# Kernel tuning notes

Measured on AMD Instinct MI355X. Metric: run time of the kernel, lower is better.

## Reference

```python
import jax, jax.numpy as jnp
from jax import lax
import numpy as np

DN = ('NHWC', 'HWIO', 'NHWC')


def conv2(x, w1, b1, w2, b2):
    # Sequential(Conv2D(units,3,same,relu), Conv2D(1,3,same,relu))
    y = jax.nn.relu(lax.conv_general_dilated(x, w1, (1, 1), 'SAME', dimension_numbers=DN) + b1)
    y = jax.nn.relu(lax.conv_general_dilated(y, w2, (1, 1), 'SAME', dimension_numbers=DN) + b2)
    return y


def resize_and_pad(fm, box, Hb, Wb):
    # Static-shape reformulation of tf.image.resize (bilinear, half-pixel) +
    # tf.pad: for every bg pixel inside the box, bilinearly sample the source
    # map; pixels outside the box are zero (the pad region).
    h, w = fm.shape[0], fm.shape[1]
    y_size = jnp.floor(Hb * (box[1] - box[0]))  # int() truncation on positives
    x_size = jnp.floor(Wb * (box[3] - box[2]))
    yf = jnp.floor(Hb * box[0])
    xf = jnp.floor(Wb * box[2])
    Y = jnp.arange(Hb, dtype=fm.dtype)[:, None]
    X = jnp.arange(Wb, dtype=fm.dtype)[None, :]
    ly = Y - yf  # local row inside resized crop
    lx = X - xf
    valid = (ly >= 0) & (ly < y_size) & (lx >= 0) & (lx < x_size)
    sy = jnp.clip((ly + 0.5) * h / jnp.maximum(y_size, 1.0) - 0.5, 0.0, h - 1.0)
    sx = jnp.clip((lx + 0.5) * w / jnp.maximum(x_size, 1.0) - 0.5, 0.0, w - 1.0)
    sy = jnp.broadcast_to(sy, (Hb, Wb))
    sx = jnp.broadcast_to(sx, (Hb, Wb))
    y0 = jnp.floor(sy).astype(jnp.int32)
    x0 = jnp.floor(sx).astype(jnp.int32)
    y1 = jnp.minimum(y0 + 1, h - 1)
    x1 = jnp.minimum(x0 + 1, w - 1)
    wy = (sy - y0.astype(fm.dtype))[..., None]
    wx = (sx - x0.astype(fm.dtype))[..., None]
    top = fm[y0, x0] * (1 - wx) + fm[y0, x1] * wx
    bot = fm[y1, x0] * (1 - wx) + fm[y1, x1] * wx
    out = top * (1 - wy) + bot * wy
    return out * valid[..., None].astype(fm.dtype)


def _forward(instance_feature, bg_feature, bbox, mrcnn_mask,
             w1i, b1i, w2i, b2i, w1b, b1b, w2b, b2b, object_n):
    B, Hi, Wi, C, M = instance_feature.shape
    Hb, Wb = bg_feature.shape[1], bg_feature.shape[2]
    # fold objects into batch for the per-instance conv
    inst = jnp.transpose(instance_feature, (0, 4, 1, 2, 3)).reshape(B * M, Hi, Wi, C)
    inst_w = conv2(inst, w1i, b1i, w2i, b2i)  # [B*M,Hi,Wi,1]
    boxes = jnp.transpose(bbox, (0, 2, 1)).reshape(B * M, 4)
    rp = lambda fm, box: resize_and_pad(fm, box, Hb, Wb)
    rw = jax.vmap(rp)(inst_w, boxes).reshape(B, M, Hb, Wb, 1)      # resized weights
    rmask = jnp.where(rw > 0, 1.0, 0.0)                              # original derives mask from weights
    rfeat = jax.vmap(rp)(inst, boxes).reshape(B, M, Hb, Wb, C)      # resized features
    bg_w = conv2(bg_feature, w1b, b1b, w2b, b2b)                     # [B,Hb,Wb,1]
    # only the first object_n[i] objects exist for image i
    valid = (jnp.arange(M)[None, :] < object_n[:, None]).astype(rw.dtype)[:, :, None, None, None]
    exp_obj = jnp.exp(rw) * rmask * valid                            # masked exp gating
    exp_bg = jnp.exp(bg_w)
    denom = exp_obj.sum(axis=1) + exp_bg                             # [B,Hb,Wb,1]
    sm_obj = (exp_obj / denom[:, None])[..., 0]                      # [B,M,Hb,Wb]
    composed = (exp_bg / denom) * bg_feature + jnp.einsum('bmhw,bmhwc->bhwc', sm_obj, rfeat)
    return composed


def setup_inputs() -> dict:
    key = jax.random.key(0)
    ks = jax.random.split(key, 16)
    B, Hi, Wi, C, M, Hb, Wb, U = 10, 64, 64, 64, 8, 128, 128, 64
    instance_feature = jax.random.normal(ks[0], (B, Hi, Wi, C, M), jnp.float32)
    bg_feature = jax.random.normal(ks[1], (B, Hb, Wb, C), jnp.float32)
    mrcnn_mask = jax.random.uniform(ks[2], (B, Hi, Wi, M), jnp.float32)
    y0 = jax.random.uniform(ks[3], (B, M), jnp.float32) * 0.4
    y1 = y0 + 0.3 + jax.random.uniform(ks[4], (B, M), jnp.float32) * 0.25
    x0 = jax.random.uniform(ks[5], (B, M), jnp.float32) * 0.4
    x1 = x0 + 0.3 + jax.random.uniform(ks[6], (B, M), jnp.float32) * 0.25
    bbox = jnp.stack([y0, y1, x0, x1], axis=1)  # [B,4,M]
    object_n = jax.random.randint(ks[7], (B,), 1, M + 1).astype(jnp.int32)
    s = 0.05
    return {
        'instance_feature': instance_feature,
        'bg_feature': bg_feature,
        'bbox': bbox,
        'mrcnn_mask': mrcnn_mask,
        'w1i': jax.random.normal(ks[8], (3, 3, C, U), jnp.float32) * s,
        'b1i': jnp.zeros((U,), jnp.float32),
        'w2i': jax.random.normal(ks[9], (3, 3, U, 1), jnp.float32) * s,
        'b2i': jnp.zeros((1,), jnp.float32),
        'w1b': jax.random.normal(ks[10], (3, 3, C, U), jnp.float32) * s,
        'b1b': jnp.zeros((U,), jnp.float32),
        'w2b': jax.random.normal(ks[11], (3, 3, U, 1), jnp.float32) * s,
        'b2b': jnp.zeros((1,), jnp.float32),
        'object_n': object_n,
    }


def reference(instance_feature, bg_feature, bbox, mrcnn_mask,
              w1i, b1i, w2i, b2i, w1b, b1b, w2b, b2b, object_n):
    return _forward(instance_feature, bg_feature, bbox, mrcnn_mask,
                    w1i, b1i, w2i, b2i, w1b, b1b, w2b, b2b, object_n)
```

## Files before the change

### kernel.cpp

```cpp
#include <hip/hip_runtime.h>
#include <cstdint>
#include <cstddef>


typedef __attribute__((ext_vector_type(8))) short short8;
typedef __attribute__((ext_vector_type(4))) float f32x4;

__device__ __forceinline__ unsigned short f2bf(float x) {
  union { float f; unsigned int u; } v; v.f = x;
  unsigned int r = (v.u + 0x7FFFu + ((v.u >> 16) & 1u)) >> 16;
  return (unsigned short)r;
}
__device__ __forceinline__ float bf2f(unsigned short h) {
  union { unsigned int u; float f; } v; v.u = ((unsigned int)h) << 16;
  return v.f;
}
__device__ __forceinline__ void split3(float v, unsigned short& h,
                                       unsigned short& m, unsigned short& l) {
  h = f2bf(v);
  float r1 = v - bf2f(h);
  m = f2bf(r1);
  float r2 = r1 - bf2f(m);
  l = f2bf(r2);
}

__global__ void prep_w3(const float* __restrict__ w, unsigned short* __restrict__ wB)
{
  int idx = blockIdx.x * 256 + threadIdx.x;
  if (idx >= 18 * 4 * 64 * 8) return;
  int i = idx & 7;
  int lane = (idx >> 3) & 63;
  int ut = (idx >> 9) & 3;
  int kc = idx >> 11;
  int k = kc * 32 + (lane >> 4) * 8 + i;
  int u = ut * 16 + (lane & 15);
  int k9 = k >> 6, c = k & 63;
  float v = w[((size_t)(k9 * 64 + c)) * 64 + u];
  unsigned short h, m, l;
  split3(v, h, m, l);
  wB[idx] = h;
  wB[36864 + idx] = m;
  wB[73728 + idx] = l;
}

__global__ __launch_bounds__(256) void tr_if(const float* __restrict__ IFh,
                                             float* __restrict__ TIF)
{
  const int idx = blockIdx.x * 256 + threadIdx.x;
  const int c = idx & 63;
  const int x = (idx >> 6) & 63;
  const int y = (idx >> 12) & 63;
  const int bb = idx >> 18;
  const float* p = IFh + (size_t)idx * 8;
  float4 v0 = *(const float4*)p;
  float4 v1 = *(const float4*)(p + 4);
  float mv[8] = {v0.x, v0.y, v0.z, v0.w, v1.x, v1.y, v1.z, v1.w};
  #pragma unroll
  for (int m = 0; m < 8; ++m)
    TIF[((size_t)(bb * 8 + m) * 4096 + y * 64 + x) * 64 + c] = mv[m];
}

__global__ __launch_bounds__(256, 2) void conv1_m(const float* __restrict__ TIF,
    const float* __restrict__ BG,
    const unsigned short* __restrict__ wBi, const unsigned short* __restrict__ wBb,
    const float* __restrict__ b1i, const float* __restrict__ b1b,
    float* __restrict__ h1i, float* __restrict__ h1g, int hh)
{
  __shared__ __align__(16) char lds[76032];

  const int tid = threadIdx.x;
  const int bid = blockIdx.x;
  const bool inst = (bid < 640);

  int H, W, imgL, xt, rg;
  const unsigned short* wB;
  const float* bias;
  const float* srcimg;
  float* dst;
  if (inst) {
    H = 64; W = 64;
    imgL = bid >> 4; rg = bid & 15; xt = 0;
    wB = wBi; bias = b1i; dst = h1i;
    srcimg = TIF + (size_t)imgL * 262144;
  } else {
    const int bb = bid - 640;
    H = 128; W = 128;
    xt = bb & 1;
    const int t2 = bb >> 1;
    rg = t2 & 31; imgL = t2 >> 5;
    wB = wBb; bias = b1b; dst = h1g;
    srcimg = BG + (size_t)(hh * 5 + imgL) * 1048576;
  }
  const int yb = rg << 2;
  const int xb = xt << 6;
  const int wave = tid >> 6, lane = tid & 63;
  const int mrow = lane & 15, g = lane >> 4;

  f32x4 z = {0.f, 0.f, 0.f, 0.f};
  f32x4 acc[4][4];
  #pragma unroll
  for (int i = 0; i < 4; ++i)
    #pragma unroll
    for (int j = 0; j < 4; ++j)
      acc[i][j] = z;

  const short8* wBp = (const short8*)wB;

  for (int cc = 0; cc < 2; ++cc) {
    if (cc) __syncthreads();
    for (int e = tid; e < 1584; e += 256) {
      const int c8 = e & 3;
      const int q = e >> 2;
      const int xi = q % 66;
      const int r = q / 66;
      const int gy = yb + r - 1;
      const int gx = xb + xi - 1;
      float v[8] = {0.f, 0.f, 0.f, 0.f, 0.f, 0.f, 0.f, 0.f};
      if (gy >= 0 && gy < H && gx >= 0 && gx < W) {
        const float* p = srcimg + ((size_t)gy * W + gx) * 64 + cc * 32 + c8 * 8;
        float4 a = *(const float4*)p;
        float4 bq = *(const float4*)(p + 4);
        v[0] = a.x; v[1] = a.y; v[2] = a.z; v[3] = a.w;
        v[4] = bq.x; v[5] = bq.y; v[6] = bq.z; v[7] = bq.w;
      }
      short8 ph, pm, pl;
      #pragma unroll
      for (int j = 0; j < 8; ++j) {
        unsigned short h2, mi, l2;
        split3(v[j], h2, mi, l2);
        ph[j] = (short)h2; pm[j] = (short)mi; pl[j] = (short)l2;
      }
      const int wbase = (r * 4 + c8) * 1056 + xi * 16;
      *(short8*)&lds[wbase] = ph;
      *(short8*)&lds[wbase + 25344] = pm;
      *(short8*)&lds[wbase + 50688] = pl;
    }
    __syncthreads();

    for (int tap = 0; tap < 9; ++tap) {
      const int dy = tap / 3, dx = tap % 3;
      const int kc = tap * 2 + cc;
      short8 a[4][3];
      #pragma unroll
      for (int pxt = 0; pxt < 4; ++pxt) {
        const int abase = ((wave + dy) * 4 + g) * 1056 + (pxt * 16 + mrow + dx) * 16;
        #pragma unroll
        for (int pl = 0; pl < 3; ++pl)
          a[pxt][pl] = *(const short8*)&lds[abase + pl * 25344];
      }
      #pragma unroll
      for (int ut = 0; ut < 4; ++ut) {
        const int bi = (kc * 4 + ut) * 64 + lane;
        short8 bfr[3];
        bfr[0] = wBp[bi];
        bfr[1] = wBp[4608 + bi];
        bfr[2] = wBp[9216 + bi];
        #pragma unroll
        for (int p = 0; p < 6; ++p) {
          const int PA[6] = {0, 0, 1, 0, 2, 1};
          const int PB[6] = {0, 1, 0, 2, 0, 1};
          const int pa = PA[p], pb = PB[p];
          #pragma unroll
          for (int pxt = 0; pxt < 4; ++pxt)
            acc[pxt][ut] = __builtin_amdgcn_mfma_f32_16x16x32_bf16(
                a[pxt][pa], bfr[pb], acc[pxt][ut], 0, 0, 0);
        }
      }
    }
  }

  const int y = yb + wave;
  #pragma unroll
  for (int ut = 0; ut < 4; ++ut) {
    const int u = ut * 16 + mrow;
    const float bv = bias[u];
    #pragma unroll
    for (int pxt = 0; pxt < 4; ++pxt) {
      #pragma unroll
      for (int r = 0; r < 4; ++r) {
        const int px = xb + pxt * 16 + g * 4 + r;
        dst[((size_t)(imgL * H + y) * W + px) * 64 + u] = fmaxf(acc[pxt][ut][r] + bv, 0.f);
      }
    }
  }
}

__global__ __launch_bounds__(256) void conv2_m(const float* __restrict__ h1i,
    const float* __restrict__ h1g,
    const float* __restrict__ w2i, const float* __restrict__ w2b,
    const float* __restrict__ b2i, const float* __restrict__ b2b,
    float* __restrict__ instw, float* __restrict__ bgw, int hh)
{
  __shared__ __align__(16) float s[18 * 18 * 36];
  __shared__ __align__(16) float wsm[576];

  const int tid = threadIdx.x;
  const int bid = blockIdx.x;
  const bool inst = (bid < 640);

  int H, W, n, xt, yt;
  const float* hsrc;
  const float* w2;
  const float* b2;
  float* dst;
  if (inst) {
    H = 64; W = 64;
    n = bid >> 4;
    const int t = bid & 15;
    xt = t & 3; yt = t >> 2;
    hsrc = h1i; w2 = w2i; b2 = b2i;
    dst = instw + (size_t)(hh * 40 + n) * 4096;
  } else {
    const int bb = bid - 640;
    H = 128; W = 128;
    n = bb >> 6;
    const int t = bb & 63;
    xt = t & 7; yt = t >> 3;
    hsrc = h1g; w2 = w2b; b2 = b2b;
    dst = bgw + (size_t)(hh * 5 + n) * 16384;
  }
  const int xb = xt << 4, yb = yt << 4;
  const int tx = tid & 15, ty = tid >> 4;

  for (int e = tid; e < 576; e += 256) wsm[e] = w2[e];

  float acc = 0.f;
  for (int cc = 0; cc < 2; ++cc) {
    const int c0 = cc << 5;
    if (cc) __syncthreads();
    for (int e = tid; e < 18 * 18 * 32; e += 256) {
      int c = e & 31;
      int p = e >> 5;
      int xx = p % 18;
      int yy = p / 18;
      int gy = yb + yy - 1, gx = xb + xx - 1;
      float v = 0.f;
      if (gy >= 0 && gy < H && gx >= 0 && gx < W)
        v = hsrc[((size_t)(n * H + gy) * W + gx) * 64 + c0 + c];
      s[(yy * 18 + xx) * 36 + c] = v;
    }
    __syncthreads();
    #pragma unroll
    for (int cq = 0; cq < 8; ++cq) {
      float4 wr[9];
      #pragma unroll
      for (int t = 0; t < 9; ++t)
        wr[t] = *(const float4*)&wsm[t * 64 + c0 + cq * 4];
      #pragma unroll
      for (int dy = 0; dy < 3; ++dy) {
        #pragma unroll
        for (int dx = 0; dx < 3; ++dx) {
          float4 iv = *(const float4*)&s[((ty + dy) * 18 + tx + dx) * 36 + cq * 4];
          float4 wv = wr[dy * 3 + dx];
          acc += iv.x * wv.x;
          acc += iv.y * wv.y;
          acc += iv.z * wv.z;
          acc += iv.w * wv.w;
        }
      }
    }
  }
  dst[(size_t)(yb + ty) * W + xb + tx] = fmaxf(acc + b2[0], 0.f);
}

__global__ __launch_bounds__(256) void compose_v4(const float* __restrict__ TIF,
    const float* __restrict__ bg, const float* __restrict__ bbox,
    const int* __restrict__ objn, const float* __restrict__ instw,
    const float* __restrict__ bgw, float* __restrict__ out, int hh)
{
  __shared__ __align__(16) float P[4][8][8];

  const int tid = threadIdx.x;
  const int lane = tid & 63;
  const int wave = tid >> 6;
  const int c = lane;
  const int pid = hh * 81920 + blockIdx.x * 4 + wave;
  const int b = pid >> 14;
  const int rem = pid & 16383;
  const int hhp = rem >> 7;
  const int www = rem & 127;

  if (lane < 8) {
    const int m = lane;
    const float y0b = bbox[b * 32 + m];
    const float y1b = bbox[b * 32 + 8 + m];
    const float x0b = bbox[b * 32 + 16 + m];
    const float x1b = bbox[b * 32 + 24 + m];
    const float ysz = floorf(128.f * (y1b - y0b));
    const float xsz = floorf(128.f * (x1b - x0b));
    const float yf = floorf(128.f * y0b);
    const float xf = floorf(128.f * x0b);
    const float ly = (float)hhp - yf;
    const float lx = (float)www - xf;
    const bool valid = (m < objn[b]) && (ly >= 0.f) && (ly < ysz)
                       && (lx >= 0.f) && (lx < xsz);
    float sy = (ly + 0.5f) * 64.f / fmaxf(ysz, 1.f) - 0.5f;
    float sx = (lx + 0.5f) * 64.f / fmaxf(xsz, 1.f) - 0.5f;
    sy = fminf(fmaxf(sy, 0.f), 63.f);
    sx = fminf(fmaxf(sx, 0.f), 63.f);
    const int y0i = (int)floorf(sy);
    const int x0i = (int)floorf(sx);
    const int y1i = min(y0i + 1, 63);
    const int x1i = min(x0i + 1, 63);
    const float wy = sy - (float)y0i;
    const float wx = sx - (float)x0i;
    const float omwx = 1.f - wx, omwy = 1.f - wy;

    const float* iw = instw + (size_t)(b * 8 + m) * 4096;
    const float v00 = iw[y0i * 64 + x0i];
    const float v01 = iw[y0i * 64 + x1i];
    const float v10 = iw[y1i * 64 + x0i];
    const float v11 = iw[y1i * 64 + x1i];
    const float rwv = (v00 * omwx + v01 * wx) * omwy + (v10 * omwx + v11 * wx) * wy;
    const bool on = valid && (rwv > 0.f);
    const float e = on ? expf(rwv) : 0.f;

    P[wave][m][0] = e;
    P[wave][m][1] = wx;
    P[wave][m][2] = wy;
    P[wave][m][3] = (float)(y0i * 4096 + x0i * 64);
    P[wave][m][4] = (float)(y0i * 4096 + x1i * 64);
    P[wave][m][5] = (float)(y1i * 4096 + x0i * 64);
    P[wave][m][6] = (float)(y1i * 4096 + x1i * 64);
    P[wave][m][7] = 0.f;
  }
  __syncthreads();

  const float ebg = expf(bgw[pid]);
  const float bgc = bg[(size_t)pid * 64 + c];
  float denom = ebg;
  float acc = ebg * bgc;
  const float* fb = TIF + (size_t)(b - hh * 5) * 8 * 262144 + c;

  #pragma unroll
  for (int m = 0; m < 8; ++m) {
    const float4 pa = *(const float4*)&P[wave][m][0];
    const float4 pb = *(const float4*)&P[wave][m][4];
    const float e = pa.x;
    denom += e;
    if (e != 0.f) {
      const float* fm = fb + (size_t)m * 262144;
      const float t00 = fm[(int)pa.w];
      const float t01 = fm[(int)pb.x];
      const float t10 = fm[(int)pb.y];
      const float t11 = fm[(int)pb.z];
      const float wx = pa.y, wy = pa.z;
      const float omwx = 1.f - wx, omwy = 1.f - wy;
      const float bil = (t00 * omwx + t01 * wx) * omwy + (t10 * omwx + t11 * wx) * wy;
      acc += e * bil;
    }
  }
  out[(size_t)pid * 64 + c] = acc / denom;
}

extern "C" void kernel_launch(void* const* d_in, const int* in_sizes, int n_in,
                              void* d_out, int out_size, void* d_ws, size_t ws_size,
                              hipStream_t stream)
{
  const float* IF   = (const float*)d_in[0];
  const float* BG   = (const float*)d_in[1];
  const float* BBOX = (const float*)d_in[2];
  const float* w1i = (const float*)d_in[4];
  const float* b1i = (const float*)d_in[5];
  const float* w2i = (const float*)d_in[6];
  const float* b2i = (const float*)d_in[7];
  const float* w1b = (const float*)d_in[8];
  const float* b1b = (const float*)d_in[9];
  const float* w2b = (const float*)d_in[10];
  const float* b2b = (const float*)d_in[11];
  const int* objn  = (const int*)d_in[12];
  float* out = (float*)d_out;

  char* wsb = (char*)d_ws;
  unsigned short* wBi3 = (unsigned short*)(wsb);
  unsigned short* wBb3 = (unsigned short*)(wsb + 221184);
  float* instw = (float*)(wsb + 442368);
  float* bgw   = (float*)(wsb + 1753088);
  float* TIF   = (float*)(wsb + 2408448);
  float* h1i   = (float*)(wsb + 44351488);
  float* h1g   = out + 5242880;

  prep_w3<<<144, 256, 0, stream>>>(w1i, wBi3);
  prep_w3<<<144, 256, 0, stream>>>(w1b, wBb3);

  for (int hh = 0; hh < 2; ++hh) {
    tr_if<<<5120, 256, 0, stream>>>(IF + (size_t)hh * 10485760, TIF);
    conv1_m<<<960, 256, 0, stream>>>(TIF, BG, wBi3, wBb3, b1i, b1b, h1i, h1g, hh);
    conv2_m<<<960, 256, 0, stream>>>(h1i, h1g, w2i, w2b, b2i, b2b, instw, bgw, hh);
    compose_v4<<<20480, 256, 0, stream>>>(TIF, BG, BBOX, objn, instw, bgw, out, hh);
  }
}
```

Measured before the change: 406.7 us.

## Prefetch second channel half into registers during first-half MFMA compute

The conv1 kernel now loads the second 32-channel half of the input tile into registers before computing on the first half, then splits it to bf16 triples and stores it to LDS after the first compute pass. The aim is to overlap global-memory latency with MFMA work instead of stalling between halves. The two weight-prep launches are merged into one kernel, and the bf16 conversion uses the library intrinsic. The prefetch buffer adds 56 floats per thread, which raises register pressure and may lower occupancy.

```diff
diff --git a/kernel.cpp b/kernel.cpp
--- a/kernel.cpp
+++ b/kernel.cpp
@@ -1,4 +1,5 @@
 #include <hip/hip_runtime.h>
+#include <hip/hip_bf16.h>
 #include <cstdint>
 #include <cstddef>
 
@@ -7,9 +8,8 @@
 typedef __attribute__((ext_vector_type(4))) float f32x4;
 
 __device__ __forceinline__ unsigned short f2bf(float x) {
-  union { float f; unsigned int u; } v; v.f = x;
-  unsigned int r = (v.u + 0x7FFFu + ((v.u >> 16) & 1u)) >> 16;
-  return (unsigned short)r;
+  __hip_bfloat16 b = __float2bfloat16(x);
+  return reinterpret_cast<unsigned short&>(b);
 }
 __device__ __forceinline__ float bf2f(unsigned short h) {
   union { unsigned int u; float f; } v; v.u = ((unsigned int)h) << 16;
@@ -24,10 +24,13 @@
   l = f2bf(r2);
 }
 
-__global__ void prep_w3(const float* __restrict__ w, unsigned short* __restrict__ wB)
-{
-  int idx = blockIdx.x * 256 + threadIdx.x;
-  if (idx >= 18 * 4 * 64 * 8) return;
+__global__ void prep_w3_2(const float* __restrict__ wA, const float* __restrict__ wBsrc,
+                          unsigned short* __restrict__ dA, unsigned short* __restrict__ dB)
+{
+  int gidx = blockIdx.x * 256 + threadIdx.x;
+  const float* w = (gidx < 36864) ? wA : wBsrc;
+  unsigned short* d = (gidx < 36864) ? dA : dB;
+  int idx = (gidx < 36864) ? gidx : gidx - 36864;
   int i = idx & 7;
   int lane = (idx >> 3) & 63;
   int ut = (idx >> 9) & 3;
@@ -38,9 +41,9 @@
   float v = w[((size_t)(k9 * 64 + c)) * 64 + u];
   unsigned short h, m, l;
   split3(v, h, m, l);
-  wB[idx] = h;
-  wB[36864 + idx] = m;
-  wB[73728 + idx] = l;
+  d[idx] = h;
+  d[36864 + idx] = m;
+  d[73728 + idx] = l;
 }
 
 __global__ __launch_bounds__(256) void tr_if(const float* __restrict__ IFh,
@@ -106,37 +109,58 @@
 
   const short8* wBp = (const short8*)wB;
 
-  for (int cc = 0; cc < 2; ++cc) {
-    if (cc) __syncthreads();
-    for (int e = tid; e < 1584; e += 256) {
+  for (int e = tid; e < 1584; e += 256) {
+    const int c8 = e & 3;
+    const int q = e >> 2;
+    const int xi = q % 66;
+    const int r = q / 66;
+    const int gy = yb + r - 1;
+    const int gx = xb + xi - 1;
+    float v[8] = {0.f, 0.f, 0.f, 0.f, 0.f, 0.f, 0.f, 0.f};
+    if (gy >= 0 && gy < H && gx >= 0 && gx < W) {
+      const float* p = srcimg + ((size_t)gy * W + gx) * 64 + c8 * 8;
+      float4 a = *(const float4*)p;
+      float4 bq = *(const float4*)(p + 4);
+      v[0] = a.x; v[1] = a.y; v[2] = a.z; v[3] = a.w;
+      v[4] = bq.x; v[5] = bq.y; v[6] = bq.z; v[7] = bq.w;
+    }
+    short8 ph, pm, pl;
+    #pragma unroll
+    for (int j = 0; j < 8; ++j) {
+      unsigned short h2, mi, l2;
+      split3(v[j], h2, mi, l2);
+      ph[j] = (short)h2; pm[j] = (short)mi; pl[j] = (short)l2;
+    }
+    const int wbase = (r * 4 + c8) * 1056 + xi * 16;
+    *(short8*)&lds[wbase] = ph;
+    *(short8*)&lds[wbase + 25344] = pm;
+    *(short8*)&lds[wbase + 50688] = pl;
+  }
+
+  float pf[7][8];
+  #pragma unroll
+  for (int it = 0; it < 7; ++it) {
+    const int e = tid + it * 256;
+    if (e < 1584) {
       const int c8 = e & 3;
       const int q = e >> 2;
       const int xi = q % 66;
       const int r = q / 66;
       const int gy = yb + r - 1;
       const int gx = xb + xi - 1;
-      float v[8] = {0.f, 0.f, 0.f, 0.f, 0.f, 0.f, 0.f, 0.f};
+      float4 a = {0.f, 0.f, 0.f, 0.f}, bq = {0.f, 0.f, 0.f, 0.f};
       if (gy >= 0 && gy < H && gx >= 0 && gx < W) {
-        const float* p = srcimg + ((size_t)gy * W + gx) * 64 + cc * 32 + c8 * 8;
-        float4 a = *(const float4*)p;
-        float4 bq = *(const float4*)(p + 4);
-        v[0] = a.x; v[1] = a.y; v[2] = a.z; v[3] = a.w;
-        v[4] = bq.x; v[5] = bq.y; v[6] = bq.z; v[7] = bq.w;
-      }
-      short8 ph, pm, pl;
-      #pragma unroll
-      for (int j = 0; j < 8; ++j) {
-        unsigned short h2, mi, l2;
-        split3(v[j], h2, mi, l2);
-        ph[j] = (short)h2; pm[j] = (short)mi; pl[j] = (short)l2;
-      }
-      const int wbase = (r * 4 + c8) * 1056 + xi * 16;
-      *(short8*)&lds[wbase] = ph;
-      *(short8*)&lds[wbase + 25344] = pm;
-      *(short8*)&lds[wbase + 50688] = pl;
-    }
-    __syncthreads();
-
+        const float* p = srcimg + ((size_t)gy * W + gx) * 64 + 32 + c8 * 8;
+        a = *(const float4*)p;
+        bq = *(const float4*)(p + 4);
+      }
+      pf[it][0] = a.x; pf[it][1] = a.y; pf[it][2] = a.z; pf[it][3] = a.w;
+      pf[it][4] = bq.x; pf[it][5] = bq.y; pf[it][6] = bq.z; pf[it][7] = bq.w;
+    }
+  }
+  __syncthreads();
+
+  auto compute = [&](int cc) {
     for (int tap = 0; tap < 9; ++tap) {
       const int dy = tap / 3, dx = tap % 3;
       const int kc = tap * 2 + cc;
@@ -167,7 +191,35 @@
         }
       }
     }
-  }
+  };
+
+  compute(0);
+  __syncthreads();
+
+  #pragma unroll
+  for (int it = 0; it < 7; ++it) {
+    const int e = tid + it * 256;
+    if (e < 1584) {
+      const int c8 = e & 3;
+      const int q = e >> 2;
+      const int xi = q % 66;
+      const int r = q / 66;
+      short8 ph, pm, pl;
+      #pragma unroll
+      for (int j = 0; j < 8; ++j) {
+        unsigned short h2, mi, l2;
+        split3(pf[it][j], h2, mi, l2);
+        ph[j] = (short)h2; pm[j] = (short)mi; pl[j] = (short)l2;
+      }
+      const int wbase = (r * 4 + c8) * 1056 + xi * 16;
+      *(short8*)&lds[wbase] = ph;
+      *(short8*)&lds[wbase + 25344] = pm;
+      *(short8*)&lds[wbase + 50688] = pl;
+    }
+  }
+  __syncthreads();
+
+  compute(1);
 
   const int y = yb + wave;
   #pragma unroll
@@ -380,8 +432,7 @@
   float* h1i   = (float*)(wsb + 44351488);
   float* h1g   = out + 5242880;
 
-  prep_w3<<<144, 256, 0, stream>>>(w1i, wBi3);
-  prep_w3<<<144, 256, 0, stream>>>(w1b, wBb3);
+  prep_w3_2<<<288, 256, 0, stream>>>(w1i, w1b, wBi3, wBb3);
 
   for (int hh = 0; hh < 2; ++hh) {
     tr_if<<<5120, 256, 0, stream>>>(IF + (size_t)hh * 10485760, TIF);
```

Result: faster. 396.5 us (-2.5%).
